# Kernel optimization log

Hardware: AMD Instinct MI355X
Metric: run time of the kernel (lower is better)

Reference implementation:

```python
import jax, jax.numpy as jnp
import numpy as np

C = 128      # channels
IN_A = 1024  # audio feature dim
IN_V = 512   # video feature dim
N = 20000    # nodes
E = 120000   # edges
NA = 10000   # number of audio nodes (placed first)
EPS = 1e-5


def _bn(h, p):
    # eval-mode BatchNorm1d: p = [gamma, beta, running_mean, running_var], each [F]
    return (h - p[2]) * jax.lax.rsqrt(p[3] + EPS) * p[0] + p[1]


def _lpp(h, bn1, W1, bn2, W2):
    # LinearPathPreact: BN -> ReLU -> Linear(no bias) -> BN -> ReLU -> Linear(no bias)
    h = jax.nn.relu(_bn(h, bn1)) @ W1.T
    h = jax.nn.relu(_bn(h, bn2)) @ W2.T
    return h


def _edge_conv(feats, src, dst, active, bn1, W1, bn2, W2, n_nodes):
    # PyG EdgeConv, aggr='max': out_i = max_{j->i} nn([x_i, x_j - x_i])
    xi = feats[dst]                      # [E, C] target features
    xj = feats[src]                      # [E, C] source features
    msg = _lpp(jnp.concatenate([xi, xj - xi], axis=-1), bn1, W1, bn2, W2)  # [E, C]
    neg = jnp.finfo(msg.dtype).min
    msg = jnp.where(active[:, None], msg, neg)  # mask out inactive edges for max
    agg = jax.ops.segment_max(msg, dst, num_segments=n_nodes)  # [N, C]
    return jnp.where(agg <= neg, jnp.zeros((), agg.dtype), agg)  # isolated nodes -> 0


def setup_inputs() -> dict:
    key = jax.random.key(0)
    ks = jax.random.split(key, 24)

    def bn_params(k, f, lead=()):
        kk = jax.random.split(k, 4)
        g = 1.0 + 0.1 * jax.random.normal(kk[0], lead + (f,), jnp.float32)
        b = 0.1 * jax.random.normal(kk[1], lead + (f,), jnp.float32)
        m = 0.1 * jax.random.normal(kk[2], lead + (f,), jnp.float32)
        v = 0.5 + jax.random.uniform(kk[3], lead + (f,), jnp.float32)
        return jnp.stack([g, b, m, v], axis=-2)  # lead + [4, f]

    inp = {}
    inp['x'] = jax.random.normal(ks[0], (N, 2, IN_A), jnp.float32)
    inp['edge_index'] = jax.random.randint(ks[1], (2, E), 0, N, dtype=jnp.int32)
    inp['edge_delta'] = jax.random.randint(ks[2], (E,), 0, 8, dtype=jnp.int32)
    inp['edge_self'] = jax.random.randint(ks[3], (E,), 0, 2, dtype=jnp.int32)
    inp['n_audio'] = NA

    s_a = (2.0 / IN_A) ** 0.5
    s_v = (2.0 / IN_V) ** 0.5
    s_2c = (2.0 / (2 * C)) ** 0.5
    s_c = (2.0 / C) ** 0.5
    inp['w0a'] = s_a * jax.random.normal(ks[4], (C, IN_A), jnp.float32)
    inp['b0a'] = 0.01 * jax.random.normal(ks[5], (C,), jnp.float32)
    inp['w0v'] = s_v * jax.random.normal(ks[6], (C, IN_V), jnp.float32)
    inp['b0v'] = 0.01 * jax.random.normal(ks[7], (C,), jnp.float32)
    inp['bn0'] = bn_params(ks[8], C)
    inp['bn_node'] = bn_params(ks[9], C, lead=(3,))          # batch_1..3: [3,4,C]
    # 8 EdgeConv MLPs in order [l1, l1t, l2, l2t, l3, l3t, l4, l4t]
    inp['ec_bn1'] = bn_params(ks[10], 2 * C, lead=(8,))      # [8,4,2C]
    inp['ec_fc1'] = s_2c * jax.random.normal(ks[11], (8, C, 2 * C), jnp.float32)
    inp['ec_bn2'] = bn_params(ks[12], C, lead=(8,))          # [8,4,C]
    inp['ec_fc2'] = s_c * jax.random.normal(ks[13], (8, C, C), jnp.float32)
    # heads: [fc, fc_a, fc_v]
    inp['w_heads'] = s_c * jax.random.normal(ks[14], (3, 2, C), jnp.float32)
    inp['b_heads'] = 0.01 * jax.random.normal(ks[15], (3, 2), jnp.float32)
    return inp


def reference(x, edge_index, edge_delta, edge_self, n_audio,
              w0a, b0a, w0v, b0v, bn0, bn_node,
              ec_bn1, ec_fc1, ec_bn2, ec_fc2, w_heads, b_heads):
    n = x.shape[0]
    src, dst = edge_index[0], edge_index[1]
    active1 = edge_delta < 1
    active2 = ((edge_delta >= 1) & (edge_delta < 4)) | (edge_self == 1)

    # layer 0: audio nodes are the first n_audio nodes (static split)
    a = x[:n_audio, 0, :IN_A] @ w0a.T + b0a          # [NA, C]
    v = x[n_audio:, 1, :IN_V] @ w0v.T + b0v          # [N-NA, C]
    g0 = jax.nn.relu(_bn(jnp.concatenate([a, v], axis=0), bn0))  # [N, C]

    def ec(f, k, act):
        return _edge_conv(f, src, dst, act, ec_bn1[k], ec_fc1[k], ec_bn2[k], ec_fc2[k], n)

    g1 = ec(ec(g0, 0, active1), 1, active2)
    g1 = jax.nn.relu(_bn(g1, bn_node[0]))            # dropout is identity (eval)
    g2 = ec(ec(g1, 2, active1), 3, active2) + g1
    g2 = jax.nn.relu(_bn(g2, bn_node[1]))
    g3 = ec(ec(g2, 4, active1), 5, active2) + g2
    g3 = jax.nn.relu(_bn(g3, bn_node[2]))
    g4 = ec(ec(g3, 6, active1), 7, active2) + g3

    out = g4 @ w_heads[0].T + b_heads[0]             # [N, 2]
    audio_out = g0[:n_audio] @ w_heads[1].T + b_heads[1]  # [NA, 2]
    video_out = g0[n_audio:] @ w_heads[2].T + b_heads[2]  # [N-NA, 2]
    return out, audio_out, video_out
```

## Files before the change

### kernel.cpp

```cpp
#include <hip/hip_runtime.h>

#define C 128
#define IN_A 1024
#define IN_V 512
#define NNODE 20000
#define NE 120000
#define NA 10000
#define NV 10000
#define EPSBN 1e-5f
#define NPAD 20032
#define EPAD 120064
#define NSTRIDE 20032

typedef __bf16 bf16_t;
typedef bf16_t bf16x8 __attribute__((ext_vector_type(8)));
typedef bf16_t bf16x2 __attribute__((ext_vector_type(2)));
typedef float f32x4 __attribute__((ext_vector_type(4)));
typedef unsigned int u32;

__device__ __forceinline__ f32x4 ld4(const float* p) {
    return *reinterpret_cast<const f32x4*>(p);
}
__device__ __forceinline__ f32x4 ld4nt(const float* p) {
    return __builtin_nontemporal_load(reinterpret_cast<const f32x4*>(p));
}

struct PB {
    const float* x;
    const int* esrc; const int* edst; const int* edelta; const int* eself;
    const float* b0a; const float* b0v;
    const float* w0a; const float* w0v;
    const float* bn0; const float* bnn;
    const float* ecb1; const float* ecf1; const float* ecb2; const float* ecf2;
    const float* wh; const float* bh;
    float* out;
    bf16_t* W16; float* SBN; int* cnts; int* indeg; int* rowst; int* curs;
    int* psrc; int* pdst;
    float* U; float* G0; float* G1; bf16_t* msg;
};

__global__ void prep0(PB P) {
    int b = blockIdx.x, t = threadIdx.x;
    if (b < 2304) {
        int i = b * 256 + t;
        float v;
        if (i < 131072) v = P.w0a[i];
        else if (i < 196608) v = P.w0v[i - 131072];
        else if (i < 458752) v = P.ecf1[i - 196608];
        else v = P.ecf2[i - 458752];
        P.W16[i] = (bf16_t)v;
    } else if (b < 2318) {
        int i = (b - 2304) * 256 + t;
        if (i >= 28 * 128) return;
        int pair = i >> 7, cc = i & 127;
        float gg, bb, mm, vv;
        if (pair == 0)      { gg = P.bn0[cc]; bb = P.bn0[128 + cc]; mm = P.bn0[256 + cc]; vv = P.bn0[384 + cc]; }
        else if (pair < 4)  { const float* q = P.bnn + (pair - 1) * 512;
                              gg = q[cc]; bb = q[128 + cc]; mm = q[256 + cc]; vv = q[384 + cc]; }
        else if (pair < 12) { const float* q = P.ecb1 + (pair - 4) * 1024;
                              gg = q[cc]; bb = q[256 + cc]; mm = q[512 + cc]; vv = q[768 + cc]; }
        else if (pair < 20) { const float* q = P.ecb1 + (pair - 12) * 1024 + 128;
                              gg = q[cc]; bb = q[256 + cc]; mm = q[512 + cc]; vv = q[768 + cc]; }
        else                { const float* q = P.ecb2 + (pair - 20) * 512;
                              gg = q[cc]; bb = q[128 + cc]; mm = q[256 + cc]; vv = q[384 + cc]; }
        float sv = gg * rsqrtf(vv + EPSBN);
        P.SBN[pair * 256 + cc] = sv;
        P.SBN[pair * 256 + 128 + cc] = bb - mm * sv;
    } else {
        int e = (b - 2318) * 256 + t;
        if (e >= NE) return;
        int d = P.edelta[e];
        int dn = P.edst[e];
        if (d < 1) atomicAdd(P.indeg + dn, 1);
        if (((d >= 1) && (d < 4)) || (P.eself[e] == 1)) atomicAdd(P.indeg + NSTRIDE + dn, 1);
    }
}

__global__ __launch_bounds__(1024) void scan_kernel(PB P) {
    __shared__ int sh[1024];
    int half = blockIdx.x;
    const int* in = P.indeg + half * NSTRIDE;
    int* rsw = P.rowst + half * NSTRIDE;
    int* cu = P.curs + half * NSTRIDE;
    int t = threadIdx.x;
    int base = t * 20;
    int s = 0;
    for (int i = 0; i < 20; i++) { int idx = base + i; if (idx < NNODE) s += in[idx]; }
    sh[t] = s;
    __syncthreads();
    for (int off = 1; off < 1024; off <<= 1) {
        int v = (t >= off) ? sh[t - off] : 0;
        __syncthreads();
        sh[t] += v;
        __syncthreads();
    }
    int run = sh[t] - s;
    for (int i = 0; i < 20; i++) {
        int idx = base + i;
        if (idx < NNODE) { int v = in[idx]; rsw[idx] = run; cu[idx] = run; run += v; }
    }
    if (t == 1023) { rsw[NNODE] = sh[1023]; P.cnts[half] = sh[1023]; }
}

__global__ __launch_bounds__(256) void combo0(PB P) {
    __shared__ __align__(16) char smem[16384];
    int b = blockIdx.x;
    if (b >= 314) {
        int e = (b - 314) * 256 + threadIdx.x;
        if (e >= NE) return;
        int d = P.edelta[e];
        int dn = P.edst[e], sn = P.esrc[e];
        if (d < 1) {
            int q = atomicAdd(P.curs + dn, 1);
            P.psrc[q] = sn; P.pdst[q] = dn;
        }
        if (((d >= 1) && (d < 4)) || (P.eself[e] == 1)) {
            int q = atomicAdd(P.curs + NSTRIDE + dn, 1);
            P.psrc[EPAD + q] = sn; P.pdst[EPAD + q] = dn;
        }
        return;
    }
    int wave = threadIdx.x >> 6, lane = threadIdx.x & 63;
    bool audio = b < 157;
    int tile = audio ? b : b - 157;
    const float* A = audio ? P.x : P.x + (size_t)NA * 2048 + 1024;
    const bf16_t* W = audio ? P.W16 : P.W16 + 131072;
    const float* bias = audio ? P.b0a : P.b0v;
    int K = audio ? IN_A : IN_V;
    int M = audio ? NA : NV;
    int nbase = audio ? 0 : NA;
    int hsel = audio ? 1 : 2;

    int m0 = tile * 64 + wave * 16;
    int arow = m0 + (lane & 15);
    int ar = arow < M ? arow : (M - 1);
    int ak = (lane >> 4) << 3;
    const float* Af = A + (size_t)ar * 2048 + ak;
    const bf16_t* Bp = W + (size_t)(lane & 15) * K + ak;

    f32x4 acc[8];
#pragma unroll
    for (int i = 0; i < 8; i++) acc[i] = (f32x4)(0.0f);
    for (int kk = 0; kk < K; kk += 32) {
        f32x4 v0 = ld4nt(Af + kk), v1 = ld4nt(Af + kk + 4);
        bf16x8 a;
#pragma unroll
        for (int j = 0; j < 4; j++) { a[j] = (bf16_t)v0[j]; a[4 + j] = (bf16_t)v1[j]; }
#pragma unroll
        for (int nt = 0; nt < 8; nt++) {
            bf16x8 bb = *reinterpret_cast<const bf16x8*>(Bp + (size_t)nt * 16 * K + kk);
            acc[nt] = __builtin_amdgcn_mfma_f32_16x16x32_bf16(a, bb, acc[nt], 0, 0, 0);
        }
    }
    int cb = lane & 15;
    float se[8], he[8], bs[8], w0[8], w1[8], s1[8], t1[8];
#pragma unroll
    for (int nt = 0; nt < 8; nt++) {
        int n = nt * 16 + cb;
        se[nt] = P.SBN[n]; he[nt] = P.SBN[128 + n]; bs[nt] = bias[n];
        w0[nt] = P.wh[hsel * 256 + n]; w1[nt] = P.wh[hsel * 256 + 128 + n];
        s1[nt] = P.SBN[4 * 256 + n]; t1[nt] = P.SBN[4 * 256 + 128 + n];
    }
    int rbase = (lane >> 4) * 4;
#pragma unroll
    for (int j = 0; j < 4; j++) {
        int m = m0 + rbase + j;
        int r = wave * 16 + rbase + j;
        float hp0 = 0.f, hp1 = 0.f;
#pragma unroll
        for (int nt = 0; nt < 8; nt++) {
            int n = nt * 16 + cb;
            float v = fmaxf((acc[nt][j] + bs[nt]) * se[nt] + he[nt], 0.0f);
            if (m < M) P.G0[(size_t)(nbase + m) * C + n] = v;
            hp0 += v * w0[nt]; hp1 += v * w1[nt];
            float av = fmaxf(v * s1[nt] + t1[nt], 0.0f);
            int byte = (r * 256 + 2 * n) ^ ((r & 7) << 4);
            *reinterpret_cast<bf16_t*>(smem + byte) = (bf16_t)av;
        }
#pragma unroll
        for (int o = 8; o; o >>= 1) { hp0 += __shfl_xor(hp0, o); hp1 += __shfl_xor(hp1, o); }
        if (cb == 0 && m < M) {
            float* op = audio ? (P.out + 40000 + (size_t)m * 2)
                              : (P.out + 60000 + (size_t)m * 2);
            op[0] = hp0 + P.bh[hsel * 2 + 0];
            op[1] = hp1 + P.bh[hsel * 2 + 1];
        }
    }
    const bf16_t* B2p = P.W16 + 196608 + (size_t)(lane & 15) * 256 + ak;
#pragma unroll
    for (int i = 0; i < 8; i++) acc[i] = (f32x4)(0.0f);
    int rr = wave * 16 + (lane & 15);
#pragma unroll
    for (int kk = 0; kk < C; kk += 32) {
        int byte = (rr * 256 + 2 * (ak + kk)) ^ ((rr & 7) << 4);
        bf16x8 a = *reinterpret_cast<const bf16x8*>(smem + byte);
#pragma unroll
        for (int nt = 0; nt < 8; nt++) {
            bf16x8 bb = *reinterpret_cast<const bf16x8*>(B2p + (size_t)nt * 16 * 256 + kk);
            acc[nt] = __builtin_amdgcn_mfma_f32_16x16x32_bf16(a, bb, acc[nt], 0, 0, 0);
        }
    }
#pragma unroll
    for (int j = 0; j < 4; j++) {
        int m = m0 + rbase + j;
        if (m >= M) continue;
#pragma unroll
        for (int nt = 0; nt < 8; nt++)
            P.U[(size_t)(nbase + m) * C + nt * 16 + cb] = acc[nt][j];
    }
}

__global__ __launch_bounds__(256) void edge_k(PB P, int h) {
    __shared__ __align__(16) float hlds[4 * 2048];
    int half = h & 1;
    int Mreal = P.cnts[half];
    int m0b = blockIdx.x * 64;
    if (m0b >= Mreal) return;
    const float* F = half ? P.G1 : P.G0;
    const int* psrc = P.psrc + (half ? EPAD : 0);
    const int* pdst = P.pdst + (half ? EPAD : 0);
    const bf16_t* B1 = P.W16 + 196608 + (size_t)h * 32768 + 128;
    const bf16_t* B2 = P.W16 + 458752 + (size_t)h * 16384;
    const float* sA = P.SBN + (12 + h) * 256; const float* shA = sA + 128;
    const float* sE = P.SBN + (20 + h) * 256; const float* shE = sE + 128;

    int wave = threadIdx.x >> 6;
    int lane = threadIdx.x & 63;
    int m0 = m0b + wave * 16;
    int arow = m0 + (lane & 15);
    int ar = arow < Mreal ? arow : (Mreal - 1);
    int ak = (lane >> 4) << 3;

    const float* Fs = F + (size_t)psrc[ar] * C + ak;
    const float* Fd = F + (size_t)pdst[ar] * C + ak;
    const bf16_t* B1p = B1 + (size_t)(lane & 15) * 256 + ak;

    f32x4 acc[8];
#pragma unroll
    for (int i = 0; i < 8; i++) acc[i] = (f32x4)(0.0f);
#pragma unroll
    for (int kk = 0; kk < C; kk += 32) {
        f32x4 vs0 = ld4(Fs + kk), vs1 = ld4(Fs + kk + 4);
        f32x4 vd0 = ld4(Fd + kk), vd1 = ld4(Fd + kk + 4);
        f32x4 s0 = ld4(sA + kk + ak), s1 = ld4(sA + kk + ak + 4);
        f32x4 h0 = ld4(shA + kk + ak), h1 = ld4(shA + kk + ak + 4);
        bf16x8 a;
#pragma unroll
        for (int j = 0; j < 4; j++) {
            float t0 = fmaxf((vs0[j] - vd0[j]) * s0[j] + h0[j], 0.0f);
            float t1 = fmaxf((vs1[j] - vd1[j]) * s1[j] + h1[j], 0.0f);
            a[j] = (bf16_t)t0; a[4 + j] = (bf16_t)t1;
        }
#pragma unroll
        for (int nt = 0; nt < 8; nt++) {
            bf16x8 bb = *reinterpret_cast<const bf16x8*>(B1p + (size_t)nt * 16 * 256 + kk);
            acc[nt] = __builtin_amdgcn_mfma_f32_16x16x32_bf16(a, bb, acc[nt], 0, 0, 0);
        }
    }
    int cb = lane & 15;
    float se[8], he[8];
#pragma unroll
    for (int nt = 0; nt < 8; nt++) { se[nt] = sE[nt * 16 + cb]; he[nt] = shE[nt * 16 + cb]; }
    int rbase = (lane >> 4) * 4;
    float* wl = hlds + wave * 2048;
#pragma unroll
    for (int j = 0; j < 4; j++) {
        int m = m0 + rbase + j;
        int mc = m < Mreal ? m : (Mreal - 1);
        const float* Ur = P.U + (size_t)pdst[mc] * C;
        int r = rbase + j;
        int sw = (r & 7) << 2;
#pragma unroll
        for (int nt = 0; nt < 8; nt++) {
            int n = nt * 16 + cb;
            float v = acc[nt][j] + Ur[n];
            wl[(r * 128 + n) ^ sw] = fmaxf(v * se[nt] + he[nt], 0.0f);
        }
    }
    const bf16_t* B2p = B2 + (size_t)(lane & 15) * C + ak;
#pragma unroll
    for (int i = 0; i < 8; i++) acc[i] = (f32x4)(0.0f);
    int rr = lane & 15;
    int swz = (rr & 7) << 2;
    const float* rl = hlds + wave * 2048;
#pragma unroll
    for (int kk = 0; kk < C; kk += 32) {
        int c0 = kk + ak;
        f32x4 v0 = *reinterpret_cast<const f32x4*>(rl + ((rr * 128 + c0) ^ swz));
        f32x4 v1 = *reinterpret_cast<const f32x4*>(rl + ((rr * 128 + c0 + 4) ^ swz));
        bf16x8 a;
#pragma unroll
        for (int j = 0; j < 4; j++) { a[j] = (bf16_t)v0[j]; a[4 + j] = (bf16_t)v1[j]; }
#pragma unroll
        for (int nt = 0; nt < 8; nt++) {
            bf16x8 bb = *reinterpret_cast<const bf16x8*>(B2p + (size_t)nt * 16 * C + kk);
            acc[nt] = __builtin_amdgcn_mfma_f32_16x16x32_bf16(a, bb, acc[nt], 0, 0, 0);
        }
    }
#pragma unroll
    for (int j = 0; j < 4; j++) {
        int m = m0 + rbase + j;
        if (m < Mreal) {
            bf16_t* op = P.msg + (size_t)m * C;
#pragma unroll
            for (int nt = 0; nt < 8; nt++) op[nt * 16 + cb] = (bf16_t)acc[nt][j];
        }
    }
}

__global__ __launch_bounds__(512) void aggk1(PB P, int h) {
    __shared__ __align__(16) char smem[4096];
    int half = h & 1, p = h >> 1;
    int tile = blockIdx.x;
    int wave = threadIdx.x >> 6;
    int lane = threadIdx.x & 63;
    const int* rs = P.rowst + half * NSTRIDE;
    const u32* msgu = (const u32*)P.msg;
    int c = lane * 2;

    const float* s1a = P.SBN + (5 + h) * 256;
    float s1c0 = s1a[c], s1c1 = s1a[c + 1], h1c0 = s1a[128 + c], h1c1 = s1a[128 + c + 1];
    float sn0 = 0.f, sn1 = 0.f, hn0 = 0.f, hn1 = 0.f;
    if (half && p < 3) {
        const float* q = P.SBN + (1 + p) * 256;
        sn0 = q[c]; sn1 = q[c + 1]; hn0 = q[128 + c]; hn1 = q[128 + c + 1];
    }
    float w0c0 = 0.f, w0c1 = 0.f, w1c0 = 0.f, w1c1 = 0.f;
    if (h == 7) { w0c0 = P.wh[c]; w0c1 = P.wh[c + 1]; w1c0 = P.wh[128 + c]; w1c1 = P.wh[129 + c]; }

#pragma unroll
    for (int i = 0; i < 2; i++) {
        int n = tile * 16 + wave * 2 + i;
        int r = wave * 2 + i;
        float a0 = 0.f, a1 = 0.f;
        if (n < NNODE) {
            int p0 = rs[n], p1 = rs[n + 1];
            float v0 = -INFINITY, v1 = -INFINITY;
            int q = p0;
            for (; q + 1 < p1; q += 2) {
                u32 u0 = msgu[(size_t)q * 64 + lane];
                u32 u1 = msgu[(size_t)(q + 1) * 64 + lane];
                v0 = fmaxf(v0, __uint_as_float(u0 << 16));
                v1 = fmaxf(v1, __uint_as_float(u0 & 0xffff0000u));
                v0 = fmaxf(v0, __uint_as_float(u1 << 16));
                v1 = fmaxf(v1, __uint_as_float(u1 & 0xffff0000u));
            }
            if (q < p1) {
                u32 u = msgu[(size_t)q * 64 + lane];
                v0 = fmaxf(v0, __uint_as_float(u << 16));
                v1 = fmaxf(v1, __uint_as_float(u & 0xffff0000u));
            }
            if (p1 == p0) { v0 = 0.f; v1 = 0.f; }
            if (h == 7) {
                float r0 = P.G0[(size_t)n * C + c], r1 = P.G0[(size_t)n * C + c + 1];
                v0 += r0; v1 += r1;
                float q0 = v0 * w0c0 + v1 * w0c1;
                float q1 = v0 * w1c0 + v1 * w1c1;
#pragma unroll
                for (int o = 32; o; o >>= 1) { q0 += __shfl_down(q0, o); q1 += __shfl_down(q1, o); }
                if (lane == 0) {
                    P.out[(size_t)n * 2 + 0] = q0 + P.bh[0];
                    P.out[(size_t)n * 2 + 1] = q1 + P.bh[1];
                }
            } else {
                float g0v, g1v;
                if (!half) {
                    g0v = v0; g1v = v1;
                    float2 w; w.x = g0v; w.y = g1v;
                    *((float2*)(P.G1 + (size_t)n * C) + lane) = w;
                } else {
                    float r0 = 0.f, r1 = 0.f;
                    if (p >= 1) { r0 = P.G0[(size_t)n * C + c]; r1 = P.G0[(size_t)n * C + c + 1]; }
                    g0v = fmaxf((v0 + r0) * sn0 + hn0, 0.0f);
                    g1v = fmaxf((v1 + r1) * sn1 + hn1, 0.0f);
                    float2 w; w.x = g0v; w.y = g1v;
                    *((float2*)(P.G0 + (size_t)n * C) + lane) = w;
                }
                a0 = fmaxf(g0v * s1c0 + h1c0, 0.0f);
                a1 = fmaxf(g1v * s1c1 + h1c1, 0.0f);
            }
        }
        if (h < 7) {
            int byte = (r * 256 + lane * 4) ^ ((r & 7) << 4);
            bf16x2 t; t[0] = (bf16_t)a0; t[1] = (bf16_t)a1;
            *reinterpret_cast<bf16x2*>(smem + byte) = t;
        }
    }
    if (h == 7) return;
    __syncthreads();
    const bf16_t* B = P.W16 + 196608 + (size_t)(h + 1) * 32768;
    int cb = lane & 15;
    int ak = (lane >> 4) << 3;
    const bf16_t* Bp = B + (size_t)(wave * 16 + cb) * 256 + ak;
    f32x4 acc = (f32x4)(0.0f);
#pragma unroll
    for (int kk = 0; kk < C; kk += 32) {
        int byte = (cb * 256 + 2 * (ak + kk)) ^ ((cb & 7) << 4);
        bf16x8 a = *reinterpret_cast<const bf16x8*>(smem + byte);
        bf16x8 bb = *reinterpret_cast<const bf16x8*>(Bp + kk);
        acc = __builtin_amdgcn_mfma_f32_16x16x32_bf16(a, bb, acc, 0, 0, 0);
    }
#pragma unroll
    for (int j = 0; j < 4; j++) {
        int m = tile * 16 + (lane >> 4) * 4 + j;
        if (m < NNODE) P.U[(size_t)m * C + wave * 16 + cb] = acc[j];
    }
}

extern "C" void kernel_launch(void* const* d_in, const int* in_sizes, int n_in,
                              void* d_out, int out_size, void* d_ws, size_t ws_size,
                              hipStream_t stream) {
    PB P;
    P.x      = (const float*)d_in[0];
    const int* eidx = (const int*)d_in[1];
    P.esrc   = eidx;
    P.edst   = eidx + NE;
    P.edelta = (const int*)d_in[2];
    P.eself  = (const int*)d_in[3];
    P.w0a    = (const float*)d_in[5];
    P.b0a    = (const float*)d_in[6];
    P.w0v    = (const float*)d_in[7];
    P.b0v    = (const float*)d_in[8];
    P.bn0    = (const float*)d_in[9];
    P.bnn    = (const float*)d_in[10];
    P.ecb1   = (const float*)d_in[11];
    P.ecf1   = (const float*)d_in[12];
    P.ecb2   = (const float*)d_in[13];
    P.ecf2   = (const float*)d_in[14];
    P.wh     = (const float*)d_in[15];
    P.bh     = (const float*)d_in[16];
    P.out    = (float*)d_out;

    char* wsb = (char*)d_ws;
    size_t off = 0;
    auto take = [&](size_t bytes) -> char* {
        char* p = wsb + off;
        off = (off + bytes + 255) & ~(size_t)255;
        return p;
    };
    P.W16   = (bf16_t*)take(589824 * 2);
    P.SBN   = (float*)take(28 * 256 * 4);
    P.cnts  = (int*)take(256);
    P.indeg = (int*)take(2 * NSTRIDE * 4);
    P.rowst = (int*)take((2 * NSTRIDE + 64) * 4);
    P.curs  = (int*)take(2 * NSTRIDE * 4);
    P.psrc  = (int*)take(2 * (size_t)EPAD * 4);
    P.pdst  = (int*)take(2 * (size_t)EPAD * 4);
    P.U     = (float*)take((size_t)NPAD * C * 4);
    P.G0    = (float*)take((size_t)NPAD * C * 4);
    P.G1    = (float*)take((size_t)NPAD * C * 4);
    P.msg   = (bf16_t*)take((size_t)EPAD * C * 2);
    (void)ws_size; (void)in_sizes; (void)n_in; (void)out_size;

    hipMemsetAsync(P.indeg, 0, 2 * NSTRIDE * 4, stream);
    prep0<<<2787, 256, 0, stream>>>(P);
    scan_kernel<<<2, 1024, 0, stream>>>(P);
    combo0<<<783, 256, 0, stream>>>(P);
    for (int h = 0; h < 8; h++) {
        edge_k<<<EPAD / 64, 256, 0, stream>>>(P, h);
        aggk1<<<1250, 512, 0, stream>>>(P, h);
    }
}
```

Before: 539.0 us.

## Store node feature buffers in bf16 and swizzle block order across XCDs

The node feature buffers G0 and G1 change from fp32 to bf16. This halves the bytes moved by the random src/dst gathers in the edge kernel and by the residual reads and writes in the aggregation kernel. A block-index remap is also added so that consecutive tiles land on the same XCD, which should improve L2 locality for edge_k and aggk1. The cost is lower precision in the residual and skip paths, since activations are now rounded to bf16 between layers.

```diff
diff --git a/kernel.cpp b/kernel.cpp
--- a/kernel.cpp
+++ b/kernel.cpp
@@ -24,6 +24,11 @@
 __device__ __forceinline__ f32x4 ld4nt(const float* p) {
     return __builtin_nontemporal_load(reinterpret_cast<const f32x4*>(p));
 }
+__device__ __forceinline__ int xcd_swz(int b, int n) {
+    int q = n >> 3, r = n & 7;
+    int x = b & 7, i = b >> 3;
+    return (x < r ? x * (q + 1) : r * (q + 1) + (x - r) * q) + i;
+}
 
 struct PB {
     const float* x;
@@ -36,7 +41,7 @@
     float* out;
     bf16_t* W16; float* SBN; int* cnts; int* indeg; int* rowst; int* curs;
     int* psrc; int* pdst;
-    float* U; float* G0; float* G1; bf16_t* msg;
+    float* U; bf16_t* G0; bf16_t* G1; bf16_t* msg;
 };
 
 __global__ void prep0(PB P) {
@@ -171,7 +176,7 @@
         for (int nt = 0; nt < 8; nt++) {
             int n = nt * 16 + cb;
             float v = fmaxf((acc[nt][j] + bs[nt]) * se[nt] + he[nt], 0.0f);
-            if (m < M) P.G0[(size_t)(nbase + m) * C + n] = v;
+            if (m < M) P.G0[(size_t)(nbase + m) * C + n] = (bf16_t)v;
             hp0 += v * w0[nt]; hp1 += v * w1[nt];
             float av = fmaxf(v * s1[nt] + t1[nt], 0.0f);
             int byte = (r * 256 + 2 * n) ^ ((r & 7) << 4);
@@ -214,9 +219,10 @@
     __shared__ __align__(16) float hlds[4 * 2048];
     int half = h & 1;
     int Mreal = P.cnts[half];
-    int m0b = blockIdx.x * 64;
-    if (m0b >= Mreal) return;
-    const float* F = half ? P.G1 : P.G0;
+    int tiles = (Mreal + 63) >> 6;
+    if ((int)blockIdx.x >= tiles) return;
+    int m0b = xcd_swz(blockIdx.x, tiles) * 64;
+    const bf16_t* F = half ? P.G1 : P.G0;
     const int* psrc = P.psrc + (half ? EPAD : 0);
     const int* pdst = P.pdst + (half ? EPAD : 0);
     const bf16_t* B1 = P.W16 + 196608 + (size_t)h * 32768 + 128;
@@ -231,8 +237,8 @@
     int ar = arow < Mreal ? arow : (Mreal - 1);
     int ak = (lane >> 4) << 3;
 
-    const float* Fs = F + (size_t)psrc[ar] * C + ak;
-    const float* Fd = F + (size_t)pdst[ar] * C + ak;
+    const bf16_t* Fs = F + (size_t)psrc[ar] * C + ak;
+    const bf16_t* Fd = F + (size_t)pdst[ar] * C + ak;
     const bf16_t* B1p = B1 + (size_t)(lane & 15) * 256 + ak;
 
     f32x4 acc[8];
@@ -240,15 +246,15 @@
     for (int i = 0; i < 8; i++) acc[i] = (f32x4)(0.0f);
 #pragma unroll
     for (int kk = 0; kk < C; kk += 32) {
-        f32x4 vs0 = ld4(Fs + kk), vs1 = ld4(Fs + kk + 4);
-        f32x4 vd0 = ld4(Fd + kk), vd1 = ld4(Fd + kk + 4);
+        bf16x8 s8 = *reinterpret_cast<const bf16x8*>(Fs + kk);
+        bf16x8 d8 = *reinterpret_cast<const bf16x8*>(Fd + kk);
         f32x4 s0 = ld4(sA + kk + ak), s1 = ld4(sA + kk + ak + 4);
         f32x4 h0 = ld4(shA + kk + ak), h1 = ld4(shA + kk + ak + 4);
         bf16x8 a;
 #pragma unroll
         for (int j = 0; j < 4; j++) {
-            float t0 = fmaxf((vs0[j] - vd0[j]) * s0[j] + h0[j], 0.0f);
-            float t1 = fmaxf((vs1[j] - vd1[j]) * s1[j] + h1[j], 0.0f);
+            float t0 = fmaxf(((float)s8[j] - (float)d8[j]) * s0[j] + h0[j], 0.0f);
+            float t1 = fmaxf(((float)s8[4 + j] - (float)d8[4 + j]) * s1[j] + h1[j], 0.0f);
             a[j] = (bf16_t)t0; a[4 + j] = (bf16_t)t1;
         }
 #pragma unroll
@@ -311,7 +317,7 @@
 __global__ __launch_bounds__(512) void aggk1(PB P, int h) {
     __shared__ __align__(16) char smem[4096];
     int half = h & 1, p = h >> 1;
-    int tile = blockIdx.x;
+    int tile = xcd_swz(blockIdx.x, 1250);
     int wave = threadIdx.x >> 6;
     int lane = threadIdx.x & 63;
     const int* rs = P.rowst + half * NSTRIDE;
@@ -352,8 +358,8 @@
             }
             if (p1 == p0) { v0 = 0.f; v1 = 0.f; }
             if (h == 7) {
-                float r0 = P.G0[(size_t)n * C + c], r1 = P.G0[(size_t)n * C + c + 1];
-                v0 += r0; v1 += r1;
+                bf16x2 r2 = *((const bf16x2*)(P.G0 + (size_t)n * C) + lane);
+                v0 += (float)r2[0]; v1 += (float)r2[1];
                 float q0 = v0 * w0c0 + v1 * w0c1;
                 float q1 = v0 * w1c0 + v1 * w1c1;
 #pragma unroll
@@ -366,15 +372,18 @@
                 float g0v, g1v;
                 if (!half) {
                     g0v = v0; g1v = v1;
-                    float2 w; w.x = g0v; w.y = g1v;
-                    *((float2*)(P.G1 + (size_t)n * C) + lane) = w;
+                    bf16x2 w; w[0] = (bf16_t)g0v; w[1] = (bf16_t)g1v;
+                    *((bf16x2*)(P.G1 + (size_t)n * C) + lane) = w;
                 } else {
                     float r0 = 0.f, r1 = 0.f;
-                    if (p >= 1) { r0 = P.G0[(size_t)n * C + c]; r1 = P.G0[(size_t)n * C + c + 1]; }
+                    if (p >= 1) {
+                        bf16x2 r2 = *((const bf16x2*)(P.G0 + (size_t)n * C) + lane);
+                        r0 = (float)r2[0]; r1 = (float)r2[1];
+                    }
                     g0v = fmaxf((v0 + r0) * sn0 + hn0, 0.0f);
                     g1v = fmaxf((v1 + r1) * sn1 + hn1, 0.0f);
-                    float2 w; w.x = g0v; w.y = g1v;
-                    *((float2*)(P.G0 + (size_t)n * C) + lane) = w;
+                    bf16x2 w; w[0] = (bf16_t)g0v; w[1] = (bf16_t)g1v;
+                    *((bf16x2*)(P.G0 + (size_t)n * C) + lane) = w;
                 }
                 a0 = fmaxf(g0v * s1c0 + h1c0, 0.0f);
                 a1 = fmaxf(g1v * s1c1 + h1c1, 0.0f);
@@ -447,8 +456,8 @@
     P.psrc  = (int*)take(2 * (size_t)EPAD * 4);
     P.pdst  = (int*)take(2 * (size_t)EPAD * 4);
     P.U     = (float*)take((size_t)NPAD * C * 4);
-    P.G0    = (float*)take((size_t)NPAD * C * 4);
-    P.G1    = (float*)take((size_t)NPAD * C * 4);
+    P.G0    = (bf16_t*)take((size_t)NPAD * C * 2);
+    P.G1    = (bf16_t*)take((size_t)NPAD * C * 2);
     P.msg   = (bf16_t*)take((size_t)EPAD * C * 2);
     (void)ws_size; (void)in_sizes; (void)n_in; (void)out_size;
 
```

Result: faster. 524.2 us (-2.8%).
